# Performance work log

Hardware: AMD Instinct MI355X
Metric: run time of the kernel (lower is better)

## Reference

```python
import jax, jax.numpy as jnp
import numpy as np

N, E, NG = 8192, 65536, 8
EMB, SH = 32, 9
HID = EMB * SH
SDIM, M, KV = 16, 2048, 16  # M = master_rate*N masters (static top-k); KV virtual nbrs/node
RMAX, NB, PC = 10.0, 8, 5
MLPD, MSH, NL = 64, 32, 3
NEMB = 10


def _radial(r):
    # r: [E,1] -> Bessel basis * polynomial cutoff envelope, [E, NB]
    x = r / RMAX
    n = jnp.arange(1, NB + 1, dtype=r.dtype)
    bes = jnp.sqrt(2.0 / RMAX) * jnp.sin(n * jnp.pi * x) / jnp.maximum(r, 1e-9)
    p = float(PC)
    env = (1.0 - (p + 1) * (p + 2) / 2 * x ** PC + p * (p + 2) * x ** (PC + 1)
           - p * (p + 1) / 2 * x ** (PC + 2))
    env = jnp.where(x < 1.0, env, 0.0)
    return bes * env


def _sph(vec):
    # component-normalized real spherical harmonics l=0,1,2 of normalized vec
    r = jnp.linalg.norm(vec, axis=-1, keepdims=True)
    u = vec / jnp.maximum(r, 1e-9)
    x, y, z = u[..., 0], u[..., 1], u[..., 2]
    s3, s5, s15 = jnp.sqrt(3.0), jnp.sqrt(5.0), jnp.sqrt(15.0)
    Y = jnp.stack([
        jnp.ones_like(x),
        s3 * y, s3 * z, s3 * x,
        s15 * x * y, s15 * y * z, 0.5 * s5 * (3 * z * z - 1.0),
        s15 * x * z, 0.5 * s15 * (x * x - y * y)], axis=-1)
    return Y, r


def _conv(h, src, dst, sh, ef, W, rw1, rb1, rw2, rb2, valid, nnodes):
    # TFN-style conv: per-edge radial MLP -> per-sh-path weights, tensor product, scatter-sum
    rad = jax.nn.relu(ef @ rw1 + rb1) @ rw2 + rb2  # [E, SH]
    coeff = sh * rad                               # [E, SH]
    h_src = h[src]                                 # gather [E, in]
    out = W.shape[-1]
    msg = jnp.zeros((src.shape[0], out), h.dtype)
    for s in range(SH):  # small fixed loop over sh paths (avoids [E,in*SH] blowup)
        msg = msg + coeff[:, s:s + 1] * (h_src @ W[:, s, :])
    if valid is not None:
        msg = msg * valid[:, None]
    return jnp.zeros((nnodes, out), h.dtype).at[dst].add(msg)


def _scatter_softmax(sc, idx, nseg):
    mx = jax.ops.segment_max(sc, idx, nseg)
    e = jnp.exp(sc - mx[idx])
    s = jax.ops.segment_sum(e, idx, nseg)
    return e / (s[idx] + 1e-9)


def _forward(atoms, pos, edge_index, batch_ids, emb_table, W0, W12,
             rw1, rb1, rw2, rb2, msw1, msb1, msw2, msb2,
             vq, vk, aw1, ab1, aw2, ab2, pw1, pb1, pw2, pb2):
    h = emb_table[atoms]
    src, dst = edge_index[0], edge_index[1]
    for i in range(NL):
        W = W0 if i == 0 else W12[i - 1]
        # ---- local message passing over original edges ----
        vec = pos[src] - pos[dst]
        sh, r = _sph(vec)
        ef = _radial(r)
        h_up = _conv(h, src, dst, sh, ef, W, rw1[i], rb1[i], rw2[i], rb2[i], None, N)
        h_local = h_up.at[:, :h.shape[-1]].add(h)  # h_update + right-pad(h)
        # ---- master selection (static top-k of soft scores, k = master_rate*N) ----
        hs = h_local[:, :SDIM]
        m = jax.nn.sigmoid((jax.nn.relu(hs @ msw1[i] + msb1[i]) @ msw2[i] + msb2[i])[:, 0])
        _, midx = jax.lax.top_k(m, M)
        midx = jnp.sort(midx)
        inv = jnp.full((N,), -1, jnp.int32).at[midx].set(jnp.arange(M, dtype=jnp.int32))
        ms, md = inv[src], inv[dst]
        vi = (ms >= 0) & (md >= 0)           # induced-subgraph edge mask
        msc = jnp.where(vi, ms, 0)
        mdc = jnp.where(vi, md, 0)
        vif = vi.astype(h.dtype)
        h_m = h_local[midx]
        pos_m = pos[midx]
        hms = h_m[:, :SDIM]
        # induced dense adjacency over masters
        adj = jnp.minimum(jnp.zeros((M, M), h.dtype).at[msc, mdc].add(vif), 1.0)
        # ---- virtual edge generation (attention over masters) ----
        S = (hms @ vq[i]) @ (hms @ vk[i]).T / jnp.sqrt(jnp.asarray(SDIM, h.dtype))
        blocked = jnp.eye(M, dtype=bool) | (adj > 0)
        S = jnp.where(blocked, -jnp.inf, S)
        A_virtual = jax.nn.softmax(S, axis=-1)
        _, tk = jax.lax.top_k(S, KV)          # top-KV virtual nbrs per master (static)
        row = jnp.repeat(jnp.arange(M), KV)
        col = tk.reshape(-1)
        sv = jnp.concatenate([row, col])      # undirected virtual edges
        dv = jnp.concatenate([col, row])
        # ---- master-level edges: induced (masked) + virtual ----
        srcm = jnp.concatenate([msc, sv])
        dstm = jnp.concatenate([mdc, dv])
        vecm = pos_m[srcm] - pos_m[dstm]
        shm, rm = _sph(vecm)
        efm = _radial(rm)
        # scatter-softmax attention weights on virtual edges
        att_in = jnp.concatenate([hms[sv], hms[dv], efm[E:]], axis=-1)
        sc = (jax.nn.relu(att_in @ aw1[i] + ab1[i]) @ aw2[i] + ab2[i])[:, 0]
        wv = _scatter_softmax(sc, dv, M)
        full_w = jnp.concatenate([vif, wv])   # induced edges weight 1 (0 if invalid)
        efm = efm * full_w[:, None]
        if i == 0:
            h_hier = h_m  # first layer: in_irreps != out_irreps -> skip master conv
        else:
            validm = jnp.concatenate([vif, jnp.ones_like(wv)])
            h_mu = _conv(h_m, srcm, dstm, shm, efm, W,
                         rw1[i], rb1[i], rw2[i], rb2[i], validm, M)
            h_hier = h_mu + h_m
        # ---- scatter masters back, soft mix ----
        h_exp = jnp.zeros_like(h_local).at[midx].set(h_hier)
        me = m[:, None]
        h = (1.0 - me) * h_local + me * h_exp
    pooled = jax.ops.segment_sum(h[:, :EMB], batch_ids, NG)  # global_add_pool
    return jax.nn.relu(pooled @ pw1 + pb1) @ pw2 + pb2


def setup_inputs() -> dict:
    key = jax.random.key(0)
    ks = jax.random.split(key, 30)
    g = lambda k, shape, s=0.1: jax.random.normal(k, shape, jnp.float32) * s
    return dict(
        atoms=jax.random.randint(ks[0], (N,), 0, NEMB),
        pos=jax.random.normal(ks[1], (N, 3), jnp.float32) * 3.0,
        edge_index=jax.random.randint(ks[2], (2, E), 0, N),
        batch_ids=jnp.sort(jax.random.randint(ks[3], (N,), 0, NG)),
        emb_table=g(ks[4], (NEMB, EMB), 1.0),
        W0=g(ks[5], (EMB, SH, HID)),
        W12=g(ks[6], (NL - 1, HID, SH, HID), 0.05),
        rw1=g(ks[7], (NL, NB, MLPD), 0.3), rb1=g(ks[8], (NL, MLPD)),
        rw2=g(ks[9], (NL, MLPD, SH), 0.3), rb2=g(ks[10], (NL, SH)),
        msw1=g(ks[11], (NL, SDIM, MSH), 0.3), msb1=g(ks[12], (NL, MSH)),
        msw2=g(ks[13], (NL, MSH, 1), 0.3), msb2=g(ks[14], (NL, 1)),
        vq=g(ks[15], (NL, SDIM, SDIM), 0.3), vk=g(ks[16], (NL, SDIM, SDIM), 0.3),
        aw1=g(ks[17], (NL, 2 * SDIM + NB, SDIM), 0.3), ab1=g(ks[18], (NL, SDIM)),
        aw2=g(ks[19], (NL, SDIM, 1), 0.3), ab2=g(ks[20], (NL, 1)),
        pw1=g(ks[21], (EMB, EMB), 0.3), pb1=g(ks[22], (EMB,)),
        pw2=g(ks[23], (EMB, 1), 0.3), pb2=g(ks[24], (1,)),
    )


def reference(atoms, pos, edge_index, batch_ids, emb_table, W0, W12,
              rw1, rb1, rw2, rb2, msw1, msb1, msw2, msb2,
              vq, vk, aw1, ab1, aw2, ab2, pw1, pb1, pw2, pb2):
    return _forward(atoms, pos, edge_index, batch_ids, emb_table, W0, W12,
                    rw1, rb1, rw2, rb2, msw1, msb1, msw2, msb2,
                    vq, vk, aw1, ab1, aw2, ab2, pw1, pb1, pw2, pb2)
```

## Files before the change

kernel.cpp:

```cpp
#include <hip/hip_runtime.h>
#include <math.h>

#define NN     8192
#define EE     65536
#define NGR    8
#define EMBD   32
#define NSH    9
#define HIDD   288
#define SD     16
#define MM     2048
#define KVK    16
#define NBAS   8
#define MLPDIM 64
#define MSHD   32
#define MK     (MM*KVK)
#define EH     (EE + 2*MK)

static __device__ __forceinline__ float relu_(float x) { return fmaxf(x, 0.f); }

__device__ __forceinline__ void radial8(float r, float ef[8]) {
  float x = r * 0.1f;
  float invr = 1.0f / fmaxf(r, 1e-9f);
  float env = 0.0f;
  if (x < 1.0f) {
    float x2 = x * x, x4 = x2 * x2, x5 = x4 * x;
    env = 1.0f - 21.0f * x5 + 35.0f * x5 * x - 15.0f * x5 * x2;
  }
  const float cst = 0.4472135954999579f;
  float a = 3.14159265358979323846f * x;
#pragma unroll
  for (int n = 1; n <= NBAS; ++n)
    ef[n - 1] = cst * sinf((float)n * a) * invr * env;
}

__device__ __forceinline__ void sph9(float vx, float vy, float vz, float Y[9], float& r) {
  r = sqrtf(vx * vx + vy * vy + vz * vz);
  float inv = 1.0f / fmaxf(r, 1e-9f);
  float x = vx * inv, y = vy * inv, z = vz * inv;
  const float s3 = 1.7320508075688772f, s5 = 2.23606797749979f, s15 = 3.872983346207417f;
  Y[0] = 1.0f;
  Y[1] = s3 * y; Y[2] = s3 * z; Y[3] = s3 * x;
  Y[4] = s15 * x * y; Y[5] = s15 * y * z;
  Y[6] = 0.5f * s5 * (3.0f * z * z - 1.0f);
  Y[7] = s15 * x * z;
  Y[8] = 0.5f * s15 * (x * x - y * y);
}

__device__ __forceinline__ void radmlp(const float ef[8], const float* w1, const float* b1,
                                       const float* w2, const float* b2, float rad[9]) {
  float z[MLPDIM];
#pragma unroll
  for (int d = 0; d < MLPDIM; ++d) {
    float a = b1[d];
#pragma unroll
    for (int b = 0; b < NBAS; ++b) a += ef[b] * w1[b * MLPDIM + d];
    z[d] = relu_(a);
  }
#pragma unroll
  for (int s = 0; s < 9; ++s) {
    float a = b2[s];
#pragma unroll
    for (int d = 0; d < MLPDIM; ++d) a += z[d] * w2[d * 9 + s];
    rad[s] = a;
  }
}

__device__ __forceinline__ unsigned int fkey(float f) {
  unsigned int u = __float_as_uint(f);
  return (u & 0x80000000u) ? ~u : (u | 0x80000000u);
}
__device__ __forceinline__ float funkey(unsigned int k) {
  unsigned int u = (k & 0x80000000u) ? (k ^ 0x80000000u) : ~k;
  return __uint_as_float(u);
}

__device__ __forceinline__ void svdv(int j, const int* __restrict__ tkb, int& s, int& d) {
  if (j < MK) { s = j / KVK; d = tkb[j]; }
  else        { int t = j - MK; s = tkb[t]; d = t / KVK; }
}
__device__ __forceinline__ int dvof(int j, const int* __restrict__ tkb) {
  return (j < MK) ? tkb[j] : (j - MK) / KVK;
}


__global__ void k_init_h(const int* __restrict__ atoms, const float* __restrict__ emb,
                         float* __restrict__ hA) {
  int t = blockIdx.x * 256 + threadIdx.x;
  int n = t / HIDD, c = t - n * HIDD;
  hA[t] = (c < EMBD) ? emb[atoms[n] * EMBD + c] : 0.0f;
}

__global__ void k_geom(const float* __restrict__ pos, const int* __restrict__ ei,
                       float* __restrict__ sh_e, float* __restrict__ ef_e) {
  int e = blockIdx.x * 256 + threadIdx.x;
  int s = ei[e], d = ei[EE + e];
  float vx = pos[s * 3] - pos[d * 3];
  float vy = pos[s * 3 + 1] - pos[d * 3 + 1];
  float vz = pos[s * 3 + 2] - pos[d * 3 + 2];
  float Y[9], r;
  sph9(vx, vy, vz, Y, r);
  float ef[8]; radial8(r, ef);
#pragma unroll
  for (int t = 0; t < 9; ++t) sh_e[e * 9 + t] = Y[t];
#pragma unroll
  for (int b = 0; b < 8; ++b) ef_e[e * 8 + b] = ef[b];
}

__global__ __launch_bounds__(256) void k_radcoeff(const float* __restrict__ ef_e,
    const float* __restrict__ sh_e, const float* __restrict__ rw1, const float* __restrict__ rb1,
    const float* __restrict__ rw2, const float* __restrict__ rb2, float* __restrict__ coeff) {
  __shared__ float w1[NBAS * MLPDIM], b1[MLPDIM], w2[MLPDIM * 9], b2[9];
  int tid = threadIdx.x;
  for (int t = tid; t < NBAS * MLPDIM; t += 256) w1[t] = rw1[t];
  for (int t = tid; t < MLPDIM * 9; t += 256) w2[t] = rw2[t];
  if (tid < MLPDIM) b1[tid] = rb1[tid];
  if (tid < 9) b2[tid] = rb2[tid];
  __syncthreads();
  int e = blockIdx.x * 256 + tid;
  float ef[8];
#pragma unroll
  for (int b = 0; b < 8; ++b) ef[b] = ef_e[e * 8 + b];
  float rad[9]; radmlp(ef, w1, b1, w2, b2, rad);
#pragma unroll
  for (int s = 0; s < 9; ++s) coeff[(size_t)e * 9 + s] = sh_e[e * 9 + s] * rad[s];
}

__global__ void k_hist(const int* __restrict__ didx, int n, int* __restrict__ cnt) {
  int e = blockIdx.x * 256 + threadIdx.x;
  if (e >= n) return;
  int d = didx[e];
  if (d >= 0) atomicAdd(&cnt[d], 1);
}
__global__ __launch_bounds__(256) void k_scan(const int* __restrict__ cnt, int* __restrict__ off,
                                              int* __restrict__ cur, int nb) {
  __shared__ int ps[257];
  int tid = threadIdx.x;
  int chunk = nb / 256;
  int s = 0;
  for (int i = 0; i < chunk; ++i) s += cnt[tid * chunk + i];
  __shared__ int part[256];
  part[tid] = s;
  __syncthreads();
  if (tid == 0) {
    int a = 0;
    for (int i = 0; i < 256; ++i) { ps[i] = a; a += part[i]; }
    ps[256] = a;
  }
  __syncthreads();
  int a = ps[tid];
  for (int i = 0; i < chunk; ++i) {
    int idx = tid * chunk + i;
    off[idx] = a; cur[idx] = a;
    a += cnt[idx];
  }
  if (tid == 255) off[nb] = a;
}
__global__ void k_scat(const int* __restrict__ didx, int n, int* __restrict__ cur,
                       int* __restrict__ elist) {
  int e = blockIdx.x * 256 + threadIdx.x;
  if (e >= n) return;
  int d = didx[e];
  if (d < 0) return;
  int pos = atomicAdd(&cur[d], 1);
  elist[pos] = e;
}

template <int NJ, int Q>
__global__ __launch_bounds__(256) void k_gatherB(const float* __restrict__ h,
    const float* __restrict__ coeff, const int* __restrict__ sidx,
    const int* __restrict__ elist, const int* __restrict__ off, float* __restrict__ G) {
  constexpr int INW = (NJ == 1) ? 32 : 288;
  constexpr int KG = INW * 9;
  constexpr int NW = 4 * Q;
  __shared__ float red[3][64][NJ * 9];
  int w = threadIdx.x >> 6, l = threadIdx.x & 63;
  int d = blockIdx.x, q = blockIdx.y;
  int e0 = off[d], e1 = off[d + 1];
  float acc[NJ][9];
#pragma unroll
  for (int j = 0; j < NJ; ++j)
#pragma unroll
    for (int s = 0; s < 9; ++s) acc[j][s] = 0.f;
  for (int p = e0 + q * 4 + w; p < e1; p += NW) {
    int e = elist[p];
    int src = sidx[e];
    const float* hr = h + (size_t)src * HIDD;
    float hv[NJ];
#pragma unroll
    for (int j = 0; j < NJ; ++j)
      hv[j] = (l + 64 * j < INW) ? hr[l + 64 * j] : 0.f;
    const float* cfp = coeff + (size_t)e * 9;
    float cf[9];
#pragma unroll
    for (int s = 0; s < 9; ++s) cf[s] = cfp[s];
#pragma unroll
    for (int j = 0; j < NJ; ++j)
#pragma unroll
      for (int s = 0; s < 9; ++s) acc[j][s] += hv[j] * cf[s];
  }
  if (w > 0) {
#pragma unroll
    for (int j = 0; j < NJ; ++j)
#pragma unroll
      for (int s = 0; s < 9; ++s) red[w - 1][l][j * 9 + s] = acc[j][s];
  }
  __syncthreads();
  if (w == 0) {
    float* Gd = G + ((size_t)q * gridDim.x + d) * KG;
#pragma unroll
    for (int j = 0; j < NJ; ++j) {
      int k = l + 64 * j;
      if (k < INW) {
#pragma unroll
        for (int s = 0; s < 9; ++s) {
          float v = acc[j][s] + red[0][l][j * 9 + s] + red[1][l][j * 9 + s] +
                    red[2][l][j * 9 + s];
          Gd[k * 9 + s] = v;
        }
      }
    }
  }
}

template <int KK, int Q>
__global__ __launch_bounds__(256) void k_gemm128(const float* __restrict__ A,
    const float* __restrict__ B, float* __restrict__ Cpart) {
  constexpr int ktiles = KK / 16;
  __shared__ float As[16][132];
  __shared__ float Bs[16][192];
  int m0 = blockIdx.x * 128, cb = blockIdx.y * 144;
  int M = gridDim.x * 128;
  size_t Astride = (size_t)M * KK;
  int Z = gridDim.z, z = blockIdx.z;
  int t0 = (z * ktiles) / Z, t1 = ((z + 1) * ktiles) / Z;
  float* C = Cpart + (size_t)z * M * 288;
  int tid = threadIdx.x;
  int rowg = tid & 15, colg = tid >> 4;
  int rA = tid >> 1, akofs = (tid & 1) * 8;
  int bkb = tid >> 4, bcg = tid & 15;
  float acc[8][9];
#pragma unroll
  for (int i = 0; i < 8; ++i)
#pragma unroll
    for (int j = 0; j < 9; ++j) acc[i][j] = 0.f;
  for (int kt = t0; kt < t1; ++kt) {
    int k0 = kt * 16;
    size_t abase = (size_t)(m0 + rA) * KK + k0 + akofs;
    float4 a0 = *(const float4*)&A[abase];
    float4 a1 = *(const float4*)&A[abase + 4];
    if constexpr (Q > 1) {
#pragma unroll
      for (int qq = 1; qq < Q; ++qq) {
        float4 t0v = *(const float4*)&A[qq * Astride + abase];
        float4 t1v = *(const float4*)&A[qq * Astride + abase + 4];
        a0.x += t0v.x; a0.y += t0v.y; a0.z += t0v.z; a0.w += t0v.w;
        a1.x += t1v.x; a1.y += t1v.y; a1.z += t1v.z; a1.w += t1v.w;
      }
    }
    float bst[9];
#pragma unroll
    for (int u = 0; u < 9; ++u)
      bst[u] = B[(size_t)(k0 + bkb) * 288 + cb + bcg * 9 + u];
    __syncthreads();
    As[akofs + 0][rA] = a0.x; As[akofs + 1][rA] = a0.y;
    As[akofs + 2][rA] = a0.z; As[akofs + 3][rA] = a0.w;
    As[akofs + 4][rA] = a1.x; As[akofs + 5][rA] = a1.y;
    As[akofs + 6][rA] = a1.z; As[akofs + 7][rA] = a1.w;
#pragma unroll
    for (int u = 0; u < 9; ++u) Bs[bkb][bcg * 12 + u] = bst[u];
    __syncthreads();
#pragma unroll
    for (int k = 0; k < 16; ++k) {
      float4 x0 = *(const float4*)&As[k][4 * rowg];
      float4 x1 = *(const float4*)&As[k][64 + 4 * rowg];
      float4 y0 = *(const float4*)&Bs[k][12 * colg];
      float4 y1 = *(const float4*)&Bs[k][12 * colg + 4];
      float y2 = Bs[k][12 * colg + 8];
      float a[8] = {x0.x, x0.y, x0.z, x0.w, x1.x, x1.y, x1.z, x1.w};
      float b[9] = {y0.x, y0.y, y0.z, y0.w, y1.x, y1.y, y1.z, y1.w, y2};
#pragma unroll
      for (int i = 0; i < 8; ++i)
#pragma unroll
        for (int j = 0; j < 9; ++j) acc[i][j] += a[i] * b[j];
    }
    __syncthreads();
  }
#pragma unroll
  for (int i = 0; i < 8; ++i) {
    int row = m0 + ((i < 4) ? (4 * rowg + i) : (64 + 4 * rowg + i - 4));
    size_t rbase = (size_t)row * 288 + cb + 9 * colg;
#pragma unroll
    for (int j = 0; j < 9; ++j) C[rbase + j] = acc[i][j];
  }
}

template <int Z>
__global__ void k_redN(const float* __restrict__ part, const float* __restrict__ hA,
                       float* __restrict__ hB, int INL) {
  int t = blockIdx.x * 256 + threadIdx.x;
  float v = 0.f;
#pragma unroll
  for (int z = 0; z < Z; ++z) v += part[(size_t)z * NN * 288 + t];
  int c = t % 288;
  if (c < INL) v += hA[t];
  hB[t] = v;
}
template <int Z>
__global__ void k_redH(const float* __restrict__ part, const float* __restrict__ hM,
                       float* __restrict__ hMu) {
  int t = blockIdx.x * 256 + threadIdx.x;
  float v = hM[t];
#pragma unroll
  for (int z = 0; z < Z; ++z) v += part[(size_t)z * MM * 288 + t];
  hMu[t] = v;
}

__global__ __launch_bounds__(256) void k_mmlp(const float* __restrict__ hB,
    const float* __restrict__ msw1, const float* __restrict__ msb1,
    const float* __restrict__ msw2, const float* __restrict__ msb2, float* __restrict__ mbuf) {
  __shared__ float w1[SD * MSHD], b1[MSHD], w2[MSHD];
  __shared__ float b2s;
  int tid = threadIdx.x;
  for (int t = tid; t < SD * MSHD; t += 256) w1[t] = msw1[t];
  if (tid < MSHD) { b1[tid] = msb1[tid]; w2[tid] = msw2[tid]; }
  if (tid == 0) b2s = msb2[0];
  __syncthreads();
  int n = blockIdx.x * 256 + tid;
  float hs[SD];
#pragma unroll
  for (int k = 0; k < SD; ++k) hs[k] = hB[(size_t)n * HIDD + k];
  float acc = b2s;
#pragma unroll
  for (int d = 0; d < MSHD; ++d) {
    float a = b1[d];
#pragma unroll
    for (int k = 0; k < SD; ++k) a += hs[k] * w1[k * MSHD + d];
    acc += relu_(a) * w2[d];
  }
  mbuf[n] = 1.0f / (1.0f + expf(-acc));
}

__global__ __launch_bounds__(256) void k_rank2(const float* __restrict__ mbuf,
                                               int* __restrict__ rankb) {
  __shared__ float vj[1024];
  __shared__ float vi_s[64];
  __shared__ int part[4][64];
  int tid = threadIdx.x;
  int i0 = blockIdx.x * 64, j0 = blockIdx.y * 1024;
  for (int t = tid; t < 1024; t += 256) vj[t] = mbuf[j0 + t];
  if (tid < 64) vi_s[tid] = mbuf[i0 + tid];
  __syncthreads();
  int il = tid & 63, js = tid >> 6;
  int i = i0 + il;
  float v = vi_s[il];
  int cnt = 0;
#pragma unroll 8
  for (int jj = js * 256; jj < js * 256 + 256; ++jj) {
    float w = vj[jj];
    cnt += (int)((w > v) | ((w == v) & (j0 + jj < i)));
  }
  part[js][il] = cnt;
  __syncthreads();
  if (tid < 64) {
    int c = part[0][tid] + part[1][tid] + part[2][tid] + part[3][tid];
    atomicAdd(&rankb[i0 + tid], c);
  }
}

__global__ __launch_bounds__(256) void k_select2(const int* __restrict__ rankb,
                                                 int* __restrict__ inv, int* __restrict__ midx) {
  __shared__ int part[256], ps[256];
  int tid = threadIdx.x;
  const int CH = NN / 256;
  int base = tid * CH;
  unsigned int mask = 0;
  int s = 0;
#pragma unroll
  for (int i = 0; i < CH; ++i) {
    int sel = (rankb[base + i] < MM) ? 1 : 0;
    mask |= (unsigned int)sel << i;
    s += sel;
  }
  part[tid] = s;
  __syncthreads();
  if (tid == 0) {
    int a = 0;
    for (int i = 0; i < 256; ++i) { ps[i] = a; a += part[i]; }
  }
  __syncthreads();
  int pos = ps[tid];
#pragma unroll
  for (int i = 0; i < CH; ++i) {
    if ((mask >> i) & 1u) {
      inv[base + i] = pos;
      midx[pos] = base + i;
      ++pos;
    } else {
      inv[base + i] = -1;
    }
  }
}

__global__ void k_gather_hm(const float* __restrict__ hB, const int* __restrict__ midx,
                            const float* __restrict__ pos, float* __restrict__ hM,
                            float* __restrict__ posm) {
  int t = blockIdx.x * 256 + threadIdx.x;
  int j = t / HIDD, c = t - j * HIDD;
  int n = midx[j];
  hM[t] = hB[(size_t)n * HIDD + c];
  if (c < 3) posm[j * 3 + c] = pos[n * 3 + c];
}

__global__ void k_qk(const float* __restrict__ hM, const float* __restrict__ vq,
                     const float* __restrict__ vk, float* __restrict__ qb, float* __restrict__ kb) {
  int g = blockIdx.x * 256 + threadIdx.x;
  int j = g >> 5, c = g & 31;
  const float* w = (c < 16) ? vq : vk;
  int cc = c & 15;
  float a = 0.f;
#pragma unroll
  for (int k = 0; k < SD; ++k) a += hM[(size_t)j * HIDD + k] * w[k * SD + cc];
  if (c < 16) qb[j * SD + cc] = a; else kb[j * SD + cc] = a;
}

__global__ __launch_bounds__(256) void k_S(const float* __restrict__ qb,
                                           const float* __restrict__ kb, float* __restrict__ S) {
  __shared__ float qs[64][17], ks[64][17];
  int r0 = blockIdx.y * 64, c0 = blockIdx.x * 64;
  int tid = threadIdx.x;
  for (int t = tid; t < 64 * 16; t += 256) {
    qs[t / 16][t % 16] = qb[(size_t)(r0 + t / 16) * SD + t % 16];
    ks[t / 16][t % 16] = kb[(size_t)(c0 + t / 16) * SD + t % 16];
  }
  __syncthreads();
  int tx = tid & 15, ty = tid >> 4;
  float acc[4][4] = {};
#pragma unroll
  for (int k = 0; k < 16; ++k) {
    float a[4], b[4];
#pragma unroll
    for (int i = 0; i < 4; ++i) a[i] = qs[ty * 4 + i][k];
#pragma unroll
    for (int j = 0; j < 4; ++j) b[j] = ks[tx * 4 + j][k];
#pragma unroll
    for (int i = 0; i < 4; ++i)
#pragma unroll
      for (int j = 0; j < 4; ++j) acc[i][j] += a[i] * b[j];
  }
#pragma unroll
  for (int i = 0; i < 4; ++i)
#pragma unroll
    for (int j = 0; j < 4; ++j) {
      int r = r0 + ty * 4 + i, c = c0 + tx * 4 + j;
      S[(size_t)r * MM + c] = (r == c) ? -INFINITY : acc[i][j] * 0.25f;
    }
}

__global__ void k_adj(const int* __restrict__ ei, const int* __restrict__ inv,
                      float* __restrict__ S) {
  int e = blockIdx.x * 256 + threadIdx.x;
  int ms = inv[ei[e]], md = inv[ei[EE + e]];
  if (ms >= 0 && md >= 0) S[(size_t)ms * MM + md] = -INFINITY;
}

__global__ __launch_bounds__(64) void k_topkv(const float* __restrict__ S, int* __restrict__ tkb) {
  int row = blockIdx.x;
  int lane = threadIdx.x;
  const float* Sr = S + (size_t)row * MM;
  float v[32];
#pragma unroll
  for (int t = 0; t < 32; ++t) v[t] = Sr[lane + 64 * t];
  unsigned int selmask = 0;
  for (int it = 0; it < KVK; ++it) {
    float best = -INFINITY;
    int bcol = 0x7fffffff;
#pragma unroll
    for (int t = 0; t < 32; ++t) {
      if (!((selmask >> t) & 1u)) {
        int c = lane + 64 * t;
        float val = v[t];
        if (val > best || (val == best && c < bcol)) { best = val; bcol = c; }
      }
    }
#pragma unroll
    for (int off = 1; off < 64; off <<= 1) {
      float ov = __shfl_xor(best, off);
      int oc = __shfl_xor(bcol, off);
      if (ov > best || (ov == best && oc < bcol)) { best = ov; bcol = oc; }
    }
    if (lane == (bcol & 63)) selmask |= 1u << (bcol >> 6);
    if (lane == 0) tkb[row * KVK + it] = bcol;
  }
}

__global__ __launch_bounds__(256) void k_att(const float* __restrict__ hM,
    const float* __restrict__ posm, const int* __restrict__ tkb,
    const float* __restrict__ aw1, const float* __restrict__ ab1,
    const float* __restrict__ aw2, const float* __restrict__ ab2, float* __restrict__ scb) {
  __shared__ float w1[40 * SD], b1[SD], w2[SD];
  __shared__ float b2s;
  int tid = threadIdx.x;
  for (int t = tid; t < 40 * SD; t += 256) w1[t] = aw1[t];
  if (tid < SD) { b1[tid] = ab1[tid]; w2[tid] = aw2[tid]; }
  if (tid == 0) b2s = ab2[0];
  __syncthreads();
  int j = blockIdx.x * 256 + tid;
  int s, d; svdv(j, tkb, s, d);
  float vx = posm[s * 3] - posm[d * 3];
  float vy = posm[s * 3 + 1] - posm[d * 3 + 1];
  float vz = posm[s * 3 + 2] - posm[d * 3 + 2];
  float r = sqrtf(vx * vx + vy * vy + vz * vz);
  float ef[8]; radial8(r, ef);
  float hsv[SD], hdv[SD];
#pragma unroll
  for (int k = 0; k < SD; ++k) { hsv[k] = hM[(size_t)s * HIDD + k]; hdv[k] = hM[(size_t)d * HIDD + k]; }
  float acc = b2s;
#pragma unroll
  for (int o = 0; o < SD; ++o) {
    float a = b1[o];
#pragma unroll
    for (int k = 0; k < SD; ++k) a += hsv[k] * w1[k * SD + o];
#pragma unroll
    for (int k = 0; k < SD; ++k) a += hdv[k] * w1[(SD + k) * SD + o];
#pragma unroll
    for (int b = 0; b < 8; ++b) a += ef[b] * w1[(2 * SD + b) * SD + o];
    acc += relu_(a) * w2[o];
  }
  scb[j] = acc;
}

__global__ void k_segmax(const float* __restrict__ scb, const int* __restrict__ tkb,
                         unsigned int* __restrict__ segmax) {
  int j = blockIdx.x * 256 + threadIdx.x;
  atomicMax(&segmax[dvof(j, tkb)], fkey(scb[j]));
}
__global__ void k_segexp(const float* __restrict__ scb, const int* __restrict__ tkb,
                         const unsigned int* __restrict__ segmax, float* __restrict__ segsum,
                         float* __restrict__ wvb) {
  int j = blockIdx.x * 256 + threadIdx.x;
  int d = dvof(j, tkb);
  float e = expf(scb[j] - funkey(segmax[d]));
  wvb[j] = e;
  atomicAdd(&segsum[d], e);
}

__global__ void k_hier_first(const int* __restrict__ ei, const int* __restrict__ inv,
                             int* __restrict__ sb, int* __restrict__ db) {
  int e = blockIdx.x * 256 + threadIdx.x;
  int ms = inv[ei[e]], md = inv[ei[EE + e]];
  bool val = (ms >= 0) && (md >= 0);
  sb[e] = val ? ms : 0;
  db[e] = val ? md : -1;
}

__global__ __launch_bounds__(256) void k_coeff_virt(const float* __restrict__ posm,
    const int* __restrict__ tkb, const float* __restrict__ wvb,
    const float* __restrict__ segsum,
    const float* __restrict__ rw1, const float* __restrict__ rb1,
    const float* __restrict__ rw2, const float* __restrict__ rb2,
    float* __restrict__ coeff, int* __restrict__ sb, int* __restrict__ db) {
  __shared__ float w1[NBAS * MLPDIM], b1[MLPDIM], w2[MLPDIM * 9], b2[9];
  int tid = threadIdx.x;
  for (int t = tid; t < NBAS * MLPDIM; t += 256) w1[t] = rw1[t];
  for (int t = tid; t < MLPDIM * 9; t += 256) w2[t] = rw2[t];
  if (tid < MLPDIM) b1[tid] = rb1[tid];
  if (tid < 9) b2[tid] = rb2[tid];
  __syncthreads();
  int j = blockIdx.x * 256 + tid;
  int s, d; svdv(j, tkb, s, d);
  float vx = posm[s * 3] - posm[d * 3];
  float vy = posm[s * 3 + 1] - posm[d * 3 + 1];
  float vz = posm[s * 3 + 2] - posm[d * 3 + 2];
  float Y[9], r;
  sph9(vx, vy, vz, Y, r);
  float ef[8]; radial8(r, ef);
  float w = wvb[j] / (segsum[d] + 1e-9f);
#pragma unroll
  for (int b = 0; b < 8; ++b) ef[b] *= w;
  float rad[9]; radmlp(ef, w1, b1, w2, b2, rad);
  int e = EE + j;
#pragma unroll
  for (int t = 0; t < 9; ++t) coeff[(size_t)e * 9 + t] = Y[t] * rad[t];
  sb[e] = s;
  db[e] = d;
}

__global__ void k_combine(const float* __restrict__ hB, const float* __restrict__ hier,
                          const float* __restrict__ mbuf, const int* __restrict__ inv,
                          float* __restrict__ hA) {
  int t = blockIdx.x * 256 + threadIdx.x;
  int n = t / HIDD;
  float f = mbuf[n];
  float v = (1.0f - f) * hB[t];
  int j = inv[n];
  if (j >= 0) v += f * hier[(size_t)j * HIDD + (t - n * HIDD)];
  hA[t] = v;
}

__global__ void k_pool(const float* __restrict__ hA, const int* __restrict__ bids,
                       float* __restrict__ pooled) {
  int t = blockIdx.x * 256 + threadIdx.x;
  int n = t / EMBD, c = t - n * EMBD;
  atomicAdd(&pooled[bids[n] * EMBD + c], hA[(size_t)n * HIDD + c]);
}

__global__ void k_head(const float* __restrict__ pooled, const float* __restrict__ pw1,
                       const float* __restrict__ pb1, const float* __restrict__ pw2,
                       const float* __restrict__ pb2, float* __restrict__ out) {
  __shared__ float z[NGR][EMBD];
  int tid = threadIdx.x;
  int g = tid / EMBD, c2 = tid % EMBD;
  if (g < NGR) {
    float a = pb1[c2];
    for (int c = 0; c < EMBD; ++c) a += pooled[g * EMBD + c] * pw1[c * EMBD + c2];
    z[g][c2] = relu_(a);
  }
  __syncthreads();
  if (tid < NGR) {
    float a = pb2[0];
    for (int c = 0; c < EMBD; ++c) a += z[tid][c] * pw2[c];
    out[tid] = a;
  }
}


extern "C" void kernel_launch(void* const* d_in, const int* in_sizes, int n_in,
                              void* d_out, int out_size, void* d_ws, size_t ws_size,
                              hipStream_t stream) {
  const int* atoms = (const int*)d_in[0];
  const float* pos = (const float*)d_in[1];
  const int* ei = (const int*)d_in[2];
  const int* bids = (const int*)d_in[3];
  const float* emb = (const float*)d_in[4];
  const float* W0 = (const float*)d_in[5];
  const float* W12 = (const float*)d_in[6];
  const float* rw1 = (const float*)d_in[7];
  const float* rb1 = (const float*)d_in[8];
  const float* rw2 = (const float*)d_in[9];
  const float* rb2 = (const float*)d_in[10];
  const float* msw1 = (const float*)d_in[11];
  const float* msb1 = (const float*)d_in[12];
  const float* msw2 = (const float*)d_in[13];
  const float* msb2 = (const float*)d_in[14];
  const float* vq = (const float*)d_in[15];
  const float* vk = (const float*)d_in[16];
  const float* aw1 = (const float*)d_in[17];
  const float* ab1 = (const float*)d_in[18];
  const float* aw2 = (const float*)d_in[19];
  const float* ab2 = (const float*)d_in[20];
  const float* pw1 = (const float*)d_in[21];
  const float* pb1 = (const float*)d_in[22];
  const float* pw2 = (const float*)d_in[23];
  const float* pb2 = (const float*)d_in[24];
  float* out = (float*)d_out;

  char* p = (char*)d_ws;
  auto alloc = [&](size_t n) { char* r = p; p += (n + 255) & ~(size_t)255; return r; };
  float* hA = (float*)alloc((size_t)NN * HIDD * 4);
  float* hB = (float*)alloc((size_t)NN * HIDD * 4);
  float* hM = (float*)alloc((size_t)MM * HIDD * 4);
  float* hMu = (float*)alloc((size_t)MM * HIDD * 4);
  float* S = (float*)alloc((size_t)MM * MM * 4);
  float* sh_e = (float*)alloc((size_t)EE * 9 * 4);
  float* ef_e = (float*)alloc((size_t)EE * 8 * 4);
  float* coeff = (float*)alloc((size_t)EH * 9 * 4);
  float* mbuf = (float*)alloc((size_t)NN * 4);
  int* rankb = (int*)alloc((size_t)NN * 4);
  int* inv = (int*)alloc((size_t)NN * 4);
  int* midx = (int*)alloc((size_t)MM * 4);
  float* posm = (float*)alloc((size_t)MM * 3 * 4);
  float* qb = (float*)alloc((size_t)MM * SD * 4);
  float* kb = (float*)alloc((size_t)MM * SD * 4);
  int* tkb = (int*)alloc((size_t)MM * KVK * 4);
  float* scb = (float*)alloc((size_t)2 * MK * 4);
  float* wvb = (float*)alloc((size_t)2 * MK * 4);
  unsigned int* segmax = (unsigned int*)alloc((size_t)MM * 4);
  float* segsum = (float*)alloc((size_t)MM * 4);
  int* sb = (int*)alloc((size_t)EH * 4);
  int* db = (int*)alloc((size_t)EH * 4);
  float* pooled = (float*)alloc((size_t)NGR * EMBD * 4);
  float* G = (float*)alloc((size_t)NN * 2592 * 4);
  float* Cpart = (float*)alloc((size_t)4 * NN * 288 * 4);
  int* cntN = (int*)alloc((size_t)NN * 4);
  int* offN = (int*)alloc((size_t)(NN + 1) * 4);
  int* curN = (int*)alloc((size_t)NN * 4);
  int* elN = (int*)alloc((size_t)EE * 4);
  int* cntH = (int*)alloc((size_t)MM * 4);
  int* offH = (int*)alloc((size_t)(MM + 1) * 4);
  int* curH = (int*)alloc((size_t)MM * 4);
  int* elH = (int*)alloc((size_t)EH * 4);

  const int* srcI = ei;
  const int* dstI = ei + EE;

  k_init_h<<<NN * HIDD / 256, 256, 0, stream>>>(atoms, emb, hA);
  k_geom<<<EE / 256, 256, 0, stream>>>(pos, ei, sh_e, ef_e);

  hipMemsetAsync(cntN, 0, NN * 4, stream);
  k_hist<<<EE / 256, 256, 0, stream>>>(dstI, EE, cntN);
  k_scan<<<1, 256, 0, stream>>>(cntN, offN, curN, NN);
  k_scat<<<EE / 256, 256, 0, stream>>>(dstI, EE, curN, elN);

  for (int L = 0; L < 3; ++L) {
    const float* W = (L == 0) ? W0 : (W12 + (size_t)(L - 1) * HIDD * 9 * HIDD);
    const float* lrw1 = rw1 + L * NBAS * MLPDIM;
    const float* lrb1 = rb1 + L * MLPDIM;
    const float* lrw2 = rw2 + L * MLPDIM * 9;
    const float* lrb2 = rb2 + L * 9;

    k_radcoeff<<<EE / 256, 256, 0, stream>>>(ef_e, sh_e, lrw1, lrb1, lrw2, lrb2, coeff);
    if (L == 0) {
      k_gatherB<1, 1><<<dim3(NN, 1), 256, 0, stream>>>(hA, coeff, srcI, elN, offN, G);
      k_gemm128<288, 1><<<dim3(NN / 128, 2, 4), 256, 0, stream>>>(G, W, Cpart);
      k_redN<4><<<NN * 288 / 256, 256, 0, stream>>>(Cpart, hA, hB, EMBD);
    } else {
      k_gatherB<5, 1><<<dim3(NN, 1), 256, 0, stream>>>(hA, coeff, srcI, elN, offN, G);
      k_gemm128<2592, 1><<<dim3(NN / 128, 2, 4), 256, 0, stream>>>(G, W, Cpart);
      k_redN<4><<<NN * 288 / 256, 256, 0, stream>>>(Cpart, hA, hB, HIDD);
    }
    k_mmlp<<<NN / 256, 256, 0, stream>>>(hB, msw1 + L * SD * MSHD, msb1 + L * MSHD,
                                         msw2 + L * MSHD, msb2 + L, mbuf);
    hipMemsetAsync(rankb, 0, NN * 4, stream);
    k_rank2<<<dim3(NN / 64, 8), 256, 0, stream>>>(mbuf, rankb);
    k_select2<<<1, 256, 0, stream>>>(rankb, inv, midx);
    k_gather_hm<<<MM * HIDD / 256, 256, 0, stream>>>(hB, midx, pos, hM, posm);

    if (L > 0) {
      k_qk<<<MM * 32 / 256, 256, 0, stream>>>(hM, vq + L * SD * SD, vk + L * SD * SD, qb, kb);
      k_S<<<dim3(MM / 64, MM / 64), 256, 0, stream>>>(qb, kb, S);
      k_adj<<<EE / 256, 256, 0, stream>>>(ei, inv, S);
      k_topkv<<<MM, 64, 0, stream>>>(S, tkb);
      k_att<<<2 * MK / 256, 256, 0, stream>>>(hM, posm, tkb, aw1 + L * 40 * SD, ab1 + L * SD,
                                              aw2 + L * SD, ab2 + L, scb);
      hipMemsetAsync(segmax, 0, MM * 4, stream);
      hipMemsetAsync(segsum, 0, MM * 4, stream);
      k_segmax<<<2 * MK / 256, 256, 0, stream>>>(scb, tkb, segmax);
      k_segexp<<<2 * MK / 256, 256, 0, stream>>>(scb, tkb, segmax, segsum, wvb);
      k_hier_first<<<EE / 256, 256, 0, stream>>>(ei, inv, sb, db);
      k_coeff_virt<<<2 * MK / 256, 256, 0, stream>>>(posm, tkb, wvb, segsum,
                                                     lrw1, lrb1, lrw2, lrb2, coeff, sb, db);
      hipMemsetAsync(cntH, 0, MM * 4, stream);
      k_hist<<<EH / 256, 256, 0, stream>>>(db, EH, cntH);
      k_scan<<<1, 256, 0, stream>>>(cntH, offH, curH, MM);
      k_scat<<<EH / 256, 256, 0, stream>>>(db, EH, curH, elH);
      k_gatherB<5, 4><<<dim3(MM, 4), 256, 0, stream>>>(hM, coeff, sb, elH, offH, G);
      k_gemm128<2592, 4><<<dim3(MM / 128, 2, 16), 256, 0, stream>>>(G, W, Cpart);
      k_redH<16><<<MM * 288 / 256, 256, 0, stream>>>(Cpart, hM, hMu);
    }
    const float* hier = (L == 0) ? hM : hMu;
    k_combine<<<NN * HIDD / 256, 256, 0, stream>>>(hB, hier, mbuf, inv, hA);
  }

  hipMemsetAsync(pooled, 0, (size_t)NGR * EMBD * 4, stream);
  k_pool<<<NN * EMBD / 256, 256, 0, stream>>>(hA, bids, pooled);
  k_head<<<1, 256, 0, stream>>>(pooled, pw1, pb1, pw2, pb2, out);
}
```

Baseline: 1.497 ms.

## Replace FP32 SIMT GEMMs with split-bf16 MFMA GEMMs (3-term hi/lo emulation)

Replaces the scalar FP32 tiled GEMM with an MFMA 16x16x32 bf16 kernel that keeps near-FP32 accuracy by splitting each operand into high and low bf16 parts and summing three products. The gather kernels now write the split bf16 hi/lo G directly, and the weights are transposed and split once per call by a new kernel. The hierarchical path adds a separate reduce-and-split pass, and the split-K factors change. This targets the compute-bound FP32 GEMMs at the cost of extra conversion passes and some precision loss from the dropped lo*lo term.

```diff
diff --git a/kernel.cpp b/kernel.cpp
--- a/kernel.cpp
+++ b/kernel.cpp
@@ -16,7 +16,19 @@
 #define MK     (MM*KVK)
 #define EH     (EE + 2*MK)
 
+typedef __attribute__((ext_vector_type(8))) short bf16x8;
+typedef __attribute__((ext_vector_type(4))) float f32x4;
+
 static __device__ __forceinline__ float relu_(float x) { return fmaxf(x, 0.f); }
+
+__device__ __forceinline__ unsigned short f2b(float f) {
+  unsigned int u = __float_as_uint(f);
+  unsigned int r = (u + 0x7FFFu + ((u >> 16) & 1u)) >> 16;
+  return (unsigned short)r;
+}
+__device__ __forceinline__ float b2f(unsigned short h) {
+  return __uint_as_float(((unsigned int)h) << 16);
+}
 
 __device__ __forceinline__ void radial8(float r, float ef[8]) {
   float x = r * 0.1f;
@@ -125,6 +137,33 @@
   for (int s = 0; s < 9; ++s) coeff[(size_t)e * 9 + s] = sh_e[e * 9 + s] * rad[s];
 }
 
+__global__ __launch_bounds__(256) void k_wt(const float* __restrict__ W, int K,
+                                            unsigned short* __restrict__ Whi,
+                                            unsigned short* __restrict__ Wlo) {
+  __shared__ unsigned short Th[32][290];
+  __shared__ unsigned short Tl[32][290];
+  int k0 = blockIdx.x * 32;
+  int tid = threadIdx.x;
+  for (int t = tid; t < 32 * 288; t += 256) {
+    int kk = t / 288, o = t % 288;
+    float wv = W[(size_t)(k0 + kk) * 288 + o];
+    unsigned short hi = f2b(wv);
+    Th[kk][o] = hi;
+    Tl[kk][o] = f2b(wv - b2f(hi));
+  }
+  __syncthreads();
+  for (int o = tid; o < 288; o += 256) {
+    unsigned short th[32], tl[32];
+#pragma unroll
+    for (int kk = 0; kk < 32; ++kk) { th[kk] = Th[kk][o]; tl[kk] = Tl[kk][o]; }
+#pragma unroll
+    for (int q = 0; q < 4; ++q) {
+      *(float4*)&Whi[(size_t)o * K + k0 + 8 * q] = *(float4*)&th[8 * q];
+      *(float4*)&Wlo[(size_t)o * K + k0 + 8 * q] = *(float4*)&tl[8 * q];
+    }
+  }
+}
+
 __global__ void k_hist(const int* __restrict__ didx, int n, int* __restrict__ cnt) {
   int e = blockIdx.x * 256 + threadIdx.x;
   if (e >= n) return;
@@ -165,13 +204,70 @@
   elist[pos] = e;
 }
 
-template <int NJ, int Q>
-__global__ __launch_bounds__(256) void k_gatherB(const float* __restrict__ h,
+template <int NJ>
+__global__ __launch_bounds__(256) void k_gatherBbf(const float* __restrict__ h,
     const float* __restrict__ coeff, const int* __restrict__ sidx,
-    const int* __restrict__ elist, const int* __restrict__ off, float* __restrict__ G) {
+    const int* __restrict__ elist, const int* __restrict__ off,
+    unsigned short* __restrict__ Ghi, unsigned short* __restrict__ Glo) {
   constexpr int INW = (NJ == 1) ? 32 : 288;
   constexpr int KG = INW * 9;
-  constexpr int NW = 4 * Q;
+  __shared__ float red[3][64][NJ * 9];
+  int w = threadIdx.x >> 6, l = threadIdx.x & 63;
+  int d = blockIdx.x;
+  int e0 = off[d], e1 = off[d + 1];
+  float acc[NJ][9];
+#pragma unroll
+  for (int j = 0; j < NJ; ++j)
+#pragma unroll
+    for (int s = 0; s < 9; ++s) acc[j][s] = 0.f;
+  for (int p = e0 + w; p < e1; p += 4) {
+    int e = elist[p];
+    int src = sidx[e];
+    const float* hr = h + (size_t)src * HIDD;
+    float hv[NJ];
+#pragma unroll
+    for (int j = 0; j < NJ; ++j)
+      hv[j] = (l + 64 * j < INW) ? hr[l + 64 * j] : 0.f;
+    const float* cfp = coeff + (size_t)e * 9;
+    float cf[9];
+#pragma unroll
+    for (int s = 0; s < 9; ++s) cf[s] = cfp[s];
+#pragma unroll
+    for (int j = 0; j < NJ; ++j)
+#pragma unroll
+      for (int s = 0; s < 9; ++s) acc[j][s] += hv[j] * cf[s];
+  }
+  if (w > 0) {
+#pragma unroll
+    for (int j = 0; j < NJ; ++j)
+#pragma unroll
+      for (int s = 0; s < 9; ++s) red[w - 1][l][j * 9 + s] = acc[j][s];
+  }
+  __syncthreads();
+  if (w == 0) {
+    unsigned short* Gdh = Ghi + (size_t)d * KG;
+    unsigned short* Gdl = Glo + (size_t)d * KG;
+#pragma unroll
+    for (int j = 0; j < NJ; ++j) {
+      int k = l + 64 * j;
+      if (k < INW) {
+#pragma unroll
+        for (int s = 0; s < 9; ++s) {
+          float v = acc[j][s] + red[0][l][j * 9 + s] + red[1][l][j * 9 + s] +
+                    red[2][l][j * 9 + s];
+          unsigned short hi = f2b(v);
+          Gdh[k * 9 + s] = hi;
+          Gdl[k * 9 + s] = f2b(v - b2f(hi));
+        }
+      }
+    }
+  }
+}
+
+__global__ __launch_bounds__(256) void k_gatherBf(const float* __restrict__ h,
+    const float* __restrict__ coeff, const int* __restrict__ sidx,
+    const int* __restrict__ elist, const int* __restrict__ off, float* __restrict__ Gf) {
+  constexpr int NJ = 5, INW = 288, KG = 2592, NW = 16;
   __shared__ float red[3][64][NJ * 9];
   int w = threadIdx.x >> 6, l = threadIdx.x & 63;
   int d = blockIdx.x, q = blockIdx.y;
@@ -206,91 +302,79 @@
   }
   __syncthreads();
   if (w == 0) {
-    float* Gd = G + ((size_t)q * gridDim.x + d) * KG;
+    float* Gd = Gf + ((size_t)q * gridDim.x + d) * KG;
 #pragma unroll
     for (int j = 0; j < NJ; ++j) {
       int k = l + 64 * j;
       if (k < INW) {
 #pragma unroll
-        for (int s = 0; s < 9; ++s) {
-          float v = acc[j][s] + red[0][l][j * 9 + s] + red[1][l][j * 9 + s] +
-                    red[2][l][j * 9 + s];
-          Gd[k * 9 + s] = v;
-        }
+        for (int s = 0; s < 9; ++s)
+          Gd[k * 9 + s] = acc[j][s] + red[0][l][j * 9 + s] + red[1][l][j * 9 + s] +
+                          red[2][l][j * 9 + s];
       }
     }
   }
 }
 
-template <int KK, int Q>
-__global__ __launch_bounds__(256) void k_gemm128(const float* __restrict__ A,
-    const float* __restrict__ B, float* __restrict__ Cpart) {
-  constexpr int ktiles = KK / 16;
-  __shared__ float As[16][132];
-  __shared__ float Bs[16][192];
-  int m0 = blockIdx.x * 128, cb = blockIdx.y * 144;
-  int M = gridDim.x * 128;
-  size_t Astride = (size_t)M * KK;
+__global__ void k_redG(const float* __restrict__ Gf, unsigned short* __restrict__ Ghi,
+                       unsigned short* __restrict__ Glo) {
+  const size_t PS = (size_t)MM * 2592;
+  size_t t = (size_t)blockIdx.x * 256 + threadIdx.x;
+  float v = Gf[t] + Gf[PS + t] + Gf[2 * PS + t] + Gf[3 * PS + t];
+  unsigned short hi = f2b(v);
+  Ghi[t] = hi;
+  Glo[t] = f2b(v - b2f(hi));
+}
+
+template <int KK>
+__global__ __launch_bounds__(256) void k_mgemm3(const unsigned short* __restrict__ Ahi,
+    const unsigned short* __restrict__ Alo,
+    const unsigned short* __restrict__ Whi, const unsigned short* __restrict__ Wlo,
+    float* __restrict__ Cpart) {
+  constexpr int slabs = KK / 32;
+  __shared__ unsigned short Bh[144 * 40];
+  __shared__ unsigned short Bl[144 * 40];
+  int m0 = blockIdx.x * 64, cb = blockIdx.y * 144;
+  int M = gridDim.x * 64;
   int Z = gridDim.z, z = blockIdx.z;
-  int t0 = (z * ktiles) / Z, t1 = ((z + 1) * ktiles) / Z;
+  int s0 = (z * slabs) / Z, s1 = ((z + 1) * slabs) / Z;
   float* C = Cpart + (size_t)z * M * 288;
   int tid = threadIdx.x;
-  int rowg = tid & 15, colg = tid >> 4;
-  int rA = tid >> 1, akofs = (tid & 1) * 8;
-  int bkb = tid >> 4, bcg = tid & 15;
-  float acc[8][9];
-#pragma unroll
-  for (int i = 0; i < 8; ++i)
-#pragma unroll
-    for (int j = 0; j < 9; ++j) acc[i][j] = 0.f;
-  for (int kt = t0; kt < t1; ++kt) {
-    int k0 = kt * 16;
-    size_t abase = (size_t)(m0 + rA) * KK + k0 + akofs;
-    float4 a0 = *(const float4*)&A[abase];
-    float4 a1 = *(const float4*)&A[abase + 4];
-    if constexpr (Q > 1) {
-#pragma unroll
-      for (int qq = 1; qq < Q; ++qq) {
-        float4 t0v = *(const float4*)&A[qq * Astride + abase];
-        float4 t1v = *(const float4*)&A[qq * Astride + abase + 4];
-        a0.x += t0v.x; a0.y += t0v.y; a0.z += t0v.z; a0.w += t0v.w;
-        a1.x += t1v.x; a1.y += t1v.y; a1.z += t1v.z; a1.w += t1v.w;
-      }
-    }
-    float bst[9];
-#pragma unroll
-    for (int u = 0; u < 9; ++u)
-      bst[u] = B[(size_t)(k0 + bkb) * 288 + cb + bcg * 9 + u];
+  int w = tid >> 6, l = tid & 63;
+  int lr = l & 15, oct = l >> 4;
+  int arow = m0 + 16 * w + lr;
+  f32x4 acc[9];
+#pragma unroll
+  for (int t = 0; t < 9; ++t) acc[t] = (f32x4){0.f, 0.f, 0.f, 0.f};
+  for (int sl = s0; sl < s1; ++sl) {
+    int k0 = sl * 32;
     __syncthreads();
-    As[akofs + 0][rA] = a0.x; As[akofs + 1][rA] = a0.y;
-    As[akofs + 2][rA] = a0.z; As[akofs + 3][rA] = a0.w;
-    As[akofs + 4][rA] = a1.x; As[akofs + 5][rA] = a1.y;
-    As[akofs + 6][rA] = a1.z; As[akofs + 7][rA] = a1.w;
-#pragma unroll
-    for (int u = 0; u < 9; ++u) Bs[bkb][bcg * 12 + u] = bst[u];
+    for (int t = tid; t < 1152; t += 256) {
+      int hsel = t / 576;
+      int qq = t - hsel * 576;
+      int c = qq >> 2, ko = qq & 3;
+      const unsigned short* Wsrc = hsel ? Wlo : Whi;
+      float4 v = *(const float4*)&Wsrc[(size_t)(cb + c) * KK + k0 + ko * 8];
+      unsigned short* Bdst = hsel ? Bl : Bh;
+      *(float4*)&Bdst[c * 40 + ko * 8] = v;
+    }
     __syncthreads();
-#pragma unroll
-    for (int k = 0; k < 16; ++k) {
-      float4 x0 = *(const float4*)&As[k][4 * rowg];
-      float4 x1 = *(const float4*)&As[k][64 + 4 * rowg];
-      float4 y0 = *(const float4*)&Bs[k][12 * colg];
-      float4 y1 = *(const float4*)&Bs[k][12 * colg + 4];
-      float y2 = Bs[k][12 * colg + 8];
-      float a[8] = {x0.x, x0.y, x0.z, x0.w, x1.x, x1.y, x1.z, x1.w};
-      float b[9] = {y0.x, y0.y, y0.z, y0.w, y1.x, y1.y, y1.z, y1.w, y2};
-#pragma unroll
-      for (int i = 0; i < 8; ++i)
-#pragma unroll
-        for (int j = 0; j < 9; ++j) acc[i][j] += a[i] * b[j];
-    }
-    __syncthreads();
-  }
-#pragma unroll
-  for (int i = 0; i < 8; ++i) {
-    int row = m0 + ((i < 4) ? (4 * rowg + i) : (64 + 4 * rowg + i - 4));
-    size_t rbase = (size_t)row * 288 + cb + 9 * colg;
-#pragma unroll
-    for (int j = 0; j < 9; ++j) C[rbase + j] = acc[i][j];
+    bf16x8 ah = *(const bf16x8*)&Ahi[(size_t)arow * KK + k0 + oct * 8];
+    bf16x8 al = *(const bf16x8*)&Alo[(size_t)arow * KK + k0 + oct * 8];
+#pragma unroll
+    for (int t = 0; t < 9; ++t) {
+      bf16x8 bh = *(const bf16x8*)&Bh[(16 * t + lr) * 40 + oct * 8];
+      bf16x8 bl = *(const bf16x8*)&Bl[(16 * t + lr) * 40 + oct * 8];
+      acc[t] = __builtin_amdgcn_mfma_f32_16x16x32_bf16(ah, bh, acc[t], 0, 0, 0);
+      acc[t] = __builtin_amdgcn_mfma_f32_16x16x32_bf16(ah, bl, acc[t], 0, 0, 0);
+      acc[t] = __builtin_amdgcn_mfma_f32_16x16x32_bf16(al, bh, acc[t], 0, 0, 0);
+    }
+  }
+#pragma unroll
+  for (int t = 0; t < 9; ++t) {
+#pragma unroll
+    for (int r = 0; r < 4; ++r)
+      C[(size_t)(m0 + 16 * w + 4 * oct + r) * 288 + cb + 16 * t + lr] = acc[t][r];
   }
 }
 
@@ -679,7 +763,18 @@
   int* sb = (int*)alloc((size_t)EH * 4);
   int* db = (int*)alloc((size_t)EH * 4);
   float* pooled = (float*)alloc((size_t)NGR * EMBD * 4);
-  float* G = (float*)alloc((size_t)NN * 2592 * 4);
+  char* Gblk = alloc((size_t)NN * 2592 * 4);
+  unsigned short* Ghi = (unsigned short*)Gblk;
+  unsigned short* Glo = Ghi + (size_t)NN * 2592;
+  float* Gf = (float*)Gblk;
+  unsigned short* Ghhi = (unsigned short*)alloc((size_t)MM * 2592 * 2);
+  unsigned short* Ghlo = (unsigned short*)alloc((size_t)MM * 2592 * 2);
+  unsigned short* Wh0 = (unsigned short*)alloc((size_t)288 * 288 * 2);
+  unsigned short* Wl0 = (unsigned short*)alloc((size_t)288 * 288 * 2);
+  unsigned short* Wh1 = (unsigned short*)alloc((size_t)2592 * 288 * 2);
+  unsigned short* Wl1 = (unsigned short*)alloc((size_t)2592 * 288 * 2);
+  unsigned short* Wh2 = (unsigned short*)alloc((size_t)2592 * 288 * 2);
+  unsigned short* Wl2 = (unsigned short*)alloc((size_t)2592 * 288 * 2);
   float* Cpart = (float*)alloc((size_t)4 * NN * 288 * 4);
   int* cntN = (int*)alloc((size_t)NN * 4);
   int* offN = (int*)alloc((size_t)(NN + 1) * 4);
@@ -696,13 +791,18 @@
   k_init_h<<<NN * HIDD / 256, 256, 0, stream>>>(atoms, emb, hA);
   k_geom<<<EE / 256, 256, 0, stream>>>(pos, ei, sh_e, ef_e);
 
+  k_wt<<<288 / 32, 256, 0, stream>>>(W0, 288, Wh0, Wl0);
+  k_wt<<<2592 / 32, 256, 0, stream>>>(W12, 2592, Wh1, Wl1);
+  k_wt<<<2592 / 32, 256, 0, stream>>>(W12 + (size_t)2592 * 288, 2592, Wh2, Wl2);
+
   hipMemsetAsync(cntN, 0, NN * 4, stream);
   k_hist<<<EE / 256, 256, 0, stream>>>(dstI, EE, cntN);
   k_scan<<<1, 256, 0, stream>>>(cntN, offN, curN, NN);
   k_scat<<<EE / 256, 256, 0, stream>>>(dstI, EE, curN, elN);
 
   for (int L = 0; L < 3; ++L) {
-    const float* W = (L == 0) ? W0 : (W12 + (size_t)(L - 1) * HIDD * 9 * HIDD);
+    const unsigned short* Wh = (L == 0) ? Wh0 : ((L == 1) ? Wh1 : Wh2);
+    const unsigned short* Wl = (L == 0) ? Wl0 : ((L == 1) ? Wl1 : Wl2);
     const float* lrw1 = rw1 + L * NBAS * MLPDIM;
     const float* lrb1 = rb1 + L * MLPDIM;
     const float* lrw2 = rw2 + L * MLPDIM * 9;
@@ -710,12 +810,12 @@
 
     k_radcoeff<<<EE / 256, 256, 0, stream>>>(ef_e, sh_e, lrw1, lrb1, lrw2, lrb2, coeff);
     if (L == 0) {
-      k_gatherB<1, 1><<<dim3(NN, 1), 256, 0, stream>>>(hA, coeff, srcI, elN, offN, G);
-      k_gemm128<288, 1><<<dim3(NN / 128, 2, 4), 256, 0, stream>>>(G, W, Cpart);
-      k_redN<4><<<NN * 288 / 256, 256, 0, stream>>>(Cpart, hA, hB, EMBD);
+      k_gatherBbf<1><<<NN, 256, 0, stream>>>(hA, coeff, srcI, elN, offN, Ghi, Glo);
+      k_mgemm3<288><<<dim3(NN / 64, 2, 2), 256, 0, stream>>>(Ghi, Glo, Wh, Wl, Cpart);
+      k_redN<2><<<NN * 288 / 256, 256, 0, stream>>>(Cpart, hA, hB, EMBD);
     } else {
-      k_gatherB<5, 1><<<dim3(NN, 1), 256, 0, stream>>>(hA, coeff, srcI, elN, offN, G);
-      k_gemm128<2592, 1><<<dim3(NN / 128, 2, 4), 256, 0, stream>>>(G, W, Cpart);
+      k_gatherBbf<5><<<NN, 256, 0, stream>>>(hA, coeff, srcI, elN, offN, Ghi, Glo);
+      k_mgemm3<2592><<<dim3(NN / 64, 2, 4), 256, 0, stream>>>(Ghi, Glo, Wh, Wl, Cpart);
       k_redN<4><<<NN * 288 / 256, 256, 0, stream>>>(Cpart, hA, hB, HIDD);
     }
     k_mmlp<<<NN / 256, 256, 0, stream>>>(hB, msw1 + L * SD * MSHD, msb1 + L * MSHD,
@@ -743,9 +843,10 @@
       k_hist<<<EH / 256, 256, 0, stream>>>(db, EH, cntH);
       k_scan<<<1, 256, 0, stream>>>(cntH, offH, curH, MM);
       k_scat<<<EH / 256, 256, 0, stream>>>(db, EH, curH, elH);
-      k_gatherB<5, 4><<<dim3(MM, 4), 256, 0, stream>>>(hM, coeff, sb, elH, offH, G);
-      k_gemm128<2592, 4><<<dim3(MM / 128, 2, 16), 256, 0, stream>>>(G, W, Cpart);
-      k_redH<16><<<MM * 288 / 256, 256, 0, stream>>>(Cpart, hM, hMu);
+      k_gatherBf<<<dim3(MM, 4), 256, 0, stream>>>(hM, coeff, sb, elH, offH, Gf);
+      k_redG<<<MM * 2592 / 256, 256, 0, stream>>>(Gf, Ghhi, Ghlo);
+      k_mgemm3<2592><<<dim3(MM / 64, 2, 8), 256, 0, stream>>>(Ghhi, Ghlo, Wh, Wl, Cpart);
+      k_redH<8><<<MM * 288 / 256, 256, 0, stream>>>(Cpart, hM, hMu);
     }
     const float* hier = (L == 0) ? hM : hMu;
     k_combine<<<NN * HIDD / 256, 256, 0, stream>>>(hB, hier, mbuf, inv, hA);
```

Measured after the change: 1.290 ms. -13.8%, faster.
